# Optimization experiments

Hardware: AMD Instinct MI355X
Metric: run time of the kernel (lower is better)

Reference implementation:

```python
import jax, jax.numpy as jnp
import numpy as np

K = 4          # torus_dim (circles)
M = 6          # n_modes
GRID = 12      # grid_size for Laplacian eigenvalues
T = 2.0        # uniformity temperature
SPREAD_W = 1.0
B = 8192       # batch size


def _karmonic_weights():
    # lambda_n = 2 - 2 cos(2 pi n / N), n = 1..M; w = (lam - lam1)/(lam_max - lam1)
    n = np.arange(1, M + 1)
    lam = 2.0 - 2.0 * np.cos(2.0 * np.pi * n / GRID)
    w = (lam - lam[0]) / (lam.max() - lam[0])
    return jnp.asarray(w, dtype=jnp.float32)


def setup_inputs() -> dict:
    key = jax.random.key(0)
    k1, k2 = jax.random.split(key)
    angles = jax.random.normal(k1, (B, K), dtype=jnp.float32)
    fourier_embed = jax.random.normal(k2, (B, 2 * K * M), dtype=jnp.float32)
    return {"angles": angles, "fourier_embed": fourier_embed}


def reference(angles, fourier_embed):
    Bn = fourier_embed.shape[0]
    w = _karmonic_weights()
    # group by mode: (B, M, 2K)
    x = fourier_embed.reshape(Bn, M, 2 * K)
    eye = jnp.eye(Bn, dtype=bool)
    log_Bm1 = jnp.log(jnp.float32(Bn - 1))

    total_unif = jnp.float32(0.0)
    mode_unifs = []
    for n in range(M):  # fixed small structural loop over modes
        xn = x[:, n, :]                                   # (B, 2K)
        sq = jnp.sum(xn * xn, axis=1)                     # (B,)
        d2 = sq[:, None] + sq[None, :] - 2.0 * (xn @ xn.T)
        d2 = jnp.maximum(d2, 0.0)                         # cdist(...)**2, clamped >= 0
        neg = jnp.where(eye, -jnp.inf, -T * d2)           # exclude diagonal like masked_select
        unif_n = jnp.mean(jax.nn.logsumexp(neg, axis=1)) - log_Bm1
        mode_unifs.append(unif_n)
        total_unif = total_unif + w[n] * unif_n

    # circular decorrelation (spread) across circle pairs, vectorized over pairs
    mu = jnp.arctan2(jnp.mean(jnp.sin(angles), axis=0),
                     jnp.mean(jnp.cos(angles), axis=0))   # (K,) circular means
    s = jnp.sin(angles - mu[None, :])                     # (B, K)
    cov = (s.T @ s) / jnp.float32(Bn)                     # (K, K) = mean(s_i * s_j)
    var = jnp.diagonal(cov)                               # mean(s_i^2)
    den = jnp.sqrt(var[:, None] * var[None, :] + 1e-8)
    corr2 = (cov / den) ** 2
    iu = np.triu_indices(K, 1)                            # upper-triangle pairs i<j
    spread = jnp.mean(corr2[iu])

    total = total_unif + jnp.float32(SPREAD_W) * spread
    return total_unif, spread, total, jnp.stack(mode_unifs)
```

## Files before the change

### kernel.cpp

```cpp
#include <hip/hip_runtime.h>
#include <math.h>

constexpr int BN = 8192;
constexpr int MN = 6;

constexpr float TL    = 2.8853900817779268f;
constexpr float SCL_Z = 2.4022448795936154f;

typedef __bf16 bf16_t;
typedef bf16_t bf16x8 __attribute__((ext_vector_type(8)));
typedef float f32x4 __attribute__((ext_vector_type(4)));

union PK { bf16_t h[8]; uint4 u; };

__device__ __forceinline__ bf16x8 frag_of(uint4 u) {
    return __builtin_bit_cast(bf16x8, u);
}

__device__ __host__ __forceinline__ int midx(int a, int b) {
    return 8 * a - (a * (a - 1)) / 2 + (b - a);
}

__global__ __launch_bounds__(256) void prep_ang(const float* __restrict__ x,
                                                const float* __restrict__ ang,
                                                uint4* __restrict__ Ap,
                                                uint4* __restrict__ Bp,
                                                float* __restrict__ angp) {
    const int blk = blockIdx.x;
    const int tid = threadIdx.x;
    if (blk < 192) {
        int idx = blk * 256 + tid;
        int n = idx >> 13;
        int j = idx & (BN - 1);
        const float* p = x + (size_t)j * 48 + n * 8;

        PK zh, zl, a3, b3;
        float sq = 0.f;
#pragma unroll
        for (int k = 0; k < 8; ++k) {
            float v = p[k];
            sq = fmaf(v, v, sq);
            float z = SCL_Z * v;
            bf16_t h = (bf16_t)z;
            zh.h[k] = h;
            zl.h[k] = (bf16_t)(z - (float)h);
        }
        float s = -TL * sq;
        bf16_t sh = (bf16_t)s;
        bf16_t sl = (bf16_t)(s - (float)sh);
        bf16_t one = (bf16_t)1.0f, zero = (bf16_t)0.0f;
        a3.h[0] = one; a3.h[1] = one; a3.h[2] = sh;  a3.h[3] = sl;
        b3.h[0] = sh;  b3.h[1] = sl;  b3.h[2] = one; b3.h[3] = one;
#pragma unroll
        for (int k = 4; k < 8; ++k) { a3.h[k] = zero; b3.h[k] = zero; }

        size_t base = ((size_t)(n * 512 + (j >> 4))) * 64 + (j & 15);
        Ap[base +  0] = zh.u;
        Ap[base + 16] = zl.u;
        Ap[base + 32] = zh.u;
        Ap[base + 48] = a3.u;
        Bp[base +  0] = zh.u;
        Bp[base + 16] = zh.u;
        Bp[base + 32] = zl.u;
        Bp[base + 48] = b3.u;
    } else {
        const int i = (blk - 192) * 256 + tid;
        float v[8];
#pragma unroll
        for (int k = 0; k < 4; ++k) __sincosf(ang[i * 4 + k], &v[k], &v[4 + k]);
        float acc[44];
        int c = 0;
#pragma unroll
        for (int a = 0; a < 8; ++a)
#pragma unroll
            for (int bq = a; bq < 8; ++bq) acc[c++] = v[a] * v[bq];
#pragma unroll
        for (int a = 0; a < 8; ++a) acc[36 + a] = v[a];

#pragma unroll
        for (int q = 0; q < 44; ++q) {
            float s = acc[q];
            s += __shfl_xor(s, 1);  s += __shfl_xor(s, 2);
            s += __shfl_xor(s, 4);  s += __shfl_xor(s, 8);
            s += __shfl_xor(s, 16); s += __shfl_xor(s, 32);
            acc[q] = s;
        }
        __shared__ float sm[4][44];
        const int w = tid >> 6, lane = tid & 63;
        if (lane == 0)
#pragma unroll
            for (int q = 0; q < 44; ++q) sm[w][q] = acc[q];
        __syncthreads();
        if (tid < 44)
            angp[(blk - 192) * 44 + tid] =
                sm[0][tid] + sm[1][tid] + sm[2][tid] + sm[3][tid];
    }
}

__global__ __launch_bounds__(512, 6) void pair_mfma(const uint4* __restrict__ Ap,
                                                    const uint4* __restrict__ Bp,
                                                    float* __restrict__ lp) {
    const int tid  = threadIdx.x;
    const int lane = tid & 63;
    const int w    = __builtin_amdgcn_readfirstlane(tid >> 6);
    const int b    = blockIdx.x;
    const int n    = b >> 7;
    const int rb   = b & 127;
    const int rb4  = rb * 4;

    bf16x8 af[4];
#pragma unroll
    for (int t = 0; t < 4; ++t)
        af[t] = frag_of(Ap[((size_t)(n * 512 + rb4 + t)) * 64 + lane]);

    float racc[16];
#pragma unroll
    for (int q = 0; q < 16; ++q) racc[q] = 0.f;

    const uint4* bbase = Bp + ((size_t)n * 512) * 64 + lane;
    const f32x4 z4 = {0.f, 0.f, 0.f, 0.f};

    const int jt0 = w * 64, jt1 = jt0 + 64;
    uint4 b0 = bbase[(size_t)jt0 * 64];
    uint4 b1 = bbase[(size_t)(jt0 + 1) * 64];
    for (int jt = jt0; jt < jt1; jt += 2) {
        uint4 p0 = bbase[(size_t)(jt + 2) * 64];
        uint4 p1 = bbase[(size_t)(jt + 3) * 64];

        f32x4 d[4];
        bf16x8 bf = frag_of(b0);
#pragma unroll
        for (int t = 0; t < 4; ++t)
            d[t] = __builtin_amdgcn_mfma_f32_16x16x32_bf16(af[t], bf, z4, 0, 0, 0);
#pragma unroll
        for (int t = 0; t < 4; ++t)
#pragma unroll
            for (int r = 0; r < 4; ++r)
                racc[t * 4 + r] += __builtin_amdgcn_exp2f(d[t][r]);

        bf = frag_of(b1);
#pragma unroll
        for (int t = 0; t < 4; ++t)
            d[t] = __builtin_amdgcn_mfma_f32_16x16x32_bf16(af[t], bf, z4, 0, 0, 0);
#pragma unroll
        for (int t = 0; t < 4; ++t)
#pragma unroll
            for (int r = 0; r < 4; ++r)
                racc[t * 4 + r] += __builtin_amdgcn_exp2f(d[t][r]);

        b0 = p0; b1 = p1;
    }

    if ((rb4 >> 6) == w) {
        const int dd = (lane & 15) - 4 * (lane >> 4);
#pragma unroll
        for (int t = 0; t < 4; ++t) {
            bf16x8 bf = frag_of(bbase[(size_t)(rb4 + t) * 64]);
            f32x4 d = __builtin_amdgcn_mfma_f32_16x16x32_bf16(af[t], bf, z4, 0, 0, 0);
#pragma unroll
            for (int r = 0; r < 4; ++r)
                if (dd == r) racc[t * 4 + r] -= __builtin_amdgcn_exp2f(d[r]);
        }
    }

#pragma unroll
    for (int q = 0; q < 16; ++q) {
        float v = racc[q];
        v += __shfl_xor(v, 1);
        v += __shfl_xor(v, 2);
        v += __shfl_xor(v, 4);
        v += __shfl_xor(v, 8);
        racc[q] = v;
    }

    __shared__ float smem[8][64];
    if ((lane & 15) == 0) {
        int g = lane >> 4;
#pragma unroll
        for (int t = 0; t < 4; ++t)
#pragma unroll
            for (int r = 0; r < 4; ++r)
                smem[w][t * 16 + g * 4 + r] = racc[t * 4 + r];
    }
    __syncthreads();

    if (tid < 64) {
        float s = 0.f;
#pragma unroll
        for (int ww = 0; ww < 8; ++ww) s += smem[ww][tid];
        float lg = logf(s);
        lg += __shfl_xor(lg, 1);
        lg += __shfl_xor(lg, 2);
        lg += __shfl_xor(lg, 4);
        lg += __shfl_xor(lg, 8);
        lg += __shfl_xor(lg, 16);
        lg += __shfl_xor(lg, 32);
        if (tid == 0) lp[b] = lg;
    }
}

__global__ __launch_bounds__(1024) void final_asm(const float* __restrict__ angp,
                                                  const float* __restrict__ lp,
                                                  float* __restrict__ out) {
    const int tid = threadIdx.x;
    __shared__ float mom[44];
    __shared__ float lds[1024];
    __shared__ float spread_s;

    if (tid < 44) {
        float s = 0.f;
        for (int bk = 0; bk < 32; ++bk) s += angp[bk * 44 + tid];
        mom[tid] = s;
    }
    __syncthreads();

    if (tid == 0) {
        float sm[4], cm[4];
#pragma unroll
        for (int k = 0; k < 4; ++k) {
            float S = mom[36 + k], C = mom[40 + k];
            float hyp = sqrtf(S * S + C * C);
            sm[k] = S / hyp;
            cm[k] = C / hyp;
        }
        auto COV = [&](int k, int l) -> float {
            int ks = k < l ? k : l, kl = k < l ? l : k;
            float mss = mom[midx(ks, kl)];
            float msc_kl = mom[midx(k, l + 4)];
            float msc_lk = mom[midx(l, k + 4)];
            float mcc = mom[midx(ks + 4, kl + 4)];
            return (cm[k] * cm[l] * mss - cm[k] * sm[l] * msc_kl -
                    sm[k] * cm[l] * msc_lk + sm[k] * sm[l] * mcc) *
                   (1.0f / (float)BN);
        };
        float var[4] = {COV(0, 0), COV(1, 1), COV(2, 2), COV(3, 3)};
        float spread = 0.f;
        const int pk[6] = {0, 0, 0, 1, 1, 2};
        const int pl[6] = {1, 2, 3, 2, 3, 3};
#pragma unroll
        for (int p = 0; p < 6; ++p) {
            float cv = COV(pk[p], pl[p]);
            float den = sqrtf(var[pk[p]] * var[pl[p]] + 1e-8f);
            float cr = cv / den;
            spread += cr * cr;
        }
        spread_s = spread * (1.0f / 6.0f);
    }

    lds[tid] = (tid < 768) ? lp[tid] : 0.f;
    __syncthreads();
    for (int off = 64; off > 0; off >>= 1) {
        if ((tid & 127) < off && tid < 768) lds[tid] += lds[tid + off];
        __syncthreads();
    }

    if (tid == 0) {
        const float wgt[6] = {0.0f, 0.19615242270663188f, 0.4641016151377544f,
                              0.7320508075688773f, 0.9282032302755088f, 1.0f};
        const float logBm1 = logf((float)(BN - 1));
        float total_unif = 0.f, unif[6];
#pragma unroll
        for (int m = 0; m < 6; ++m) {
            unif[m] = lds[m * 128] * (1.0f / (float)BN) - logBm1;
            total_unif += wgt[m] * unif[m];
        }
        out[0] = total_unif;
        out[1] = spread_s;
        out[2] = total_unif + spread_s;
#pragma unroll
        for (int m = 0; m < 6; ++m) out[3 + m] = unif[m];
    }
}

extern "C" void kernel_launch(void* const* d_in, const int* in_sizes, int n_in,
                              void* d_out, int out_size, void* d_ws, size_t ws_size,
                              hipStream_t stream) {
    const float* angles  = (const float*)d_in[0];
    const float* fourier = (const float*)d_in[1];
    float* out = (float*)d_out;

    char* ws = (char*)d_ws;
    uint4* Bp   = (uint4*)(ws + 0);
    uint4* Ap   = (uint4*)(ws + 3145728);
    float* lp   = (float*)(ws + 6291456);
    float* angp = (float*)(ws + 6294528);

    prep_ang<<<dim3(224), dim3(256), 0, stream>>>(fourier, angles, Ap, Bp, angp);
    pair_mfma<<<dim3(MN * 128), dim3(512), 0, stream>>>(Ap, Bp, lp);
    final_asm<<<dim3(1), dim3(1024), 0, stream>>>(angp, lp, out);
}
```

Before: 60.37 us.

## Split pair kernel column range in half across two blocks, add log reduction kernel

Doubles the pair_mfma grid by giving each block half of the column tiles, interleaved with stride 16 across waves. Partial row sums go to a workspace, and a new log_red kernel adds the two halves, takes the log and reduces. The aim is better CU occupancy and load balance: 1536 blocks instead of 768, with launch bounds raised to 8 waves per SIMD. The cost is an extra kernel launch and a global round trip for the partial sums.

New measurement: 204.6 us. 3.39x slower.

```diff
diff --git a/kernel.cpp b/kernel.cpp
--- a/kernel.cpp
+++ b/kernel.cpp
@@ -97,16 +97,18 @@
     }
 }
 
-__global__ __launch_bounds__(512, 6) void pair_mfma(const uint4* __restrict__ Ap,
+__global__ __launch_bounds__(512, 8) void pair_mfma(const uint4* __restrict__ Ap,
                                                     const uint4* __restrict__ Bp,
-                                                    float* __restrict__ lp) {
+                                                    float* __restrict__ Sh) {
     const int tid  = threadIdx.x;
     const int lane = tid & 63;
     const int w    = __builtin_amdgcn_readfirstlane(tid >> 6);
     const int b    = blockIdx.x;
-    const int n    = b >> 7;
-    const int rb   = b & 127;
+    const int n    = b >> 8;
+    const int rb   = (b >> 1) & 127;
+    const int h    = b & 1;
     const int rb4  = rb * 4;
+    const int base = 2 * w + h;
 
     bf16x8 af[4];
 #pragma unroll
@@ -120,41 +122,41 @@
     const uint4* bbase = Bp + ((size_t)n * 512) * 64 + lane;
     const f32x4 z4 = {0.f, 0.f, 0.f, 0.f};
 
-    const int jt0 = w * 64, jt1 = jt0 + 64;
-    uint4 b0 = bbase[(size_t)jt0 * 64];
-    uint4 b1 = bbase[(size_t)(jt0 + 1) * 64];
-    for (int jt = jt0; jt < jt1; jt += 2) {
-        uint4 p0 = bbase[(size_t)(jt + 2) * 64];
-        uint4 p1 = bbase[(size_t)(jt + 3) * 64];
-
-        f32x4 d[4];
-        bf16x8 bf = frag_of(b0);
-#pragma unroll
-        for (int t = 0; t < 4; ++t)
-            d[t] = __builtin_amdgcn_mfma_f32_16x16x32_bf16(af[t], bf, z4, 0, 0, 0);
+    uint4 b0 = bbase[(size_t)base * 64];
+    uint4 b1 = bbase[(size_t)(base + 16) * 64];
+    for (int m = 0; m < 16; ++m) {
+        const int jtA = base + 32 * m;
+        uint4 p0 = bbase[(size_t)(jtA + 32) * 64];
+        uint4 p1 = bbase[(size_t)(jtA + 48) * 64];
+
+        bf16x8 bfA = frag_of(b0);
+        bf16x8 bfB = frag_of(b1);
+        f32x4 d0[4], d1[4];
+#pragma unroll
+        for (int t = 0; t < 4; ++t)
+            d0[t] = __builtin_amdgcn_mfma_f32_16x16x32_bf16(af[t], bfA, z4, 0, 0, 0);
+#pragma unroll
+        for (int t = 0; t < 4; ++t)
+            d1[t] = __builtin_amdgcn_mfma_f32_16x16x32_bf16(af[t], bfB, z4, 0, 0, 0);
 #pragma unroll
         for (int t = 0; t < 4; ++t)
 #pragma unroll
             for (int r = 0; r < 4; ++r)
-                racc[t * 4 + r] += __builtin_amdgcn_exp2f(d[t][r]);
-
-        bf = frag_of(b1);
-#pragma unroll
-        for (int t = 0; t < 4; ++t)
-            d[t] = __builtin_amdgcn_mfma_f32_16x16x32_bf16(af[t], bf, z4, 0, 0, 0);
+                racc[t * 4 + r] += __builtin_amdgcn_exp2f(d0[t][r]);
 #pragma unroll
         for (int t = 0; t < 4; ++t)
 #pragma unroll
             for (int r = 0; r < 4; ++r)
-                racc[t * 4 + r] += __builtin_amdgcn_exp2f(d[t][r]);
+                racc[t * 4 + r] += __builtin_amdgcn_exp2f(d1[t][r]);
 
         b0 = p0; b1 = p1;
     }
 
-    if ((rb4 >> 6) == w) {
-        const int dd = (lane & 15) - 4 * (lane >> 4);
-#pragma unroll
-        for (int t = 0; t < 4; ++t) {
+#pragma unroll
+    for (int t = 0; t < 4; ++t) {
+        const int rel = rb4 + t - base;
+        if (rel >= 0 && (rel & 15) == 0) {
+            const int dd = (lane & 15) - 4 * (lane >> 4);
             bf16x8 bf = frag_of(bbase[(size_t)(rb4 + t) * 64]);
             f32x4 d = __builtin_amdgcn_mfma_f32_16x16x32_bf16(af[t], bf, z4, 0, 0, 0);
 #pragma unroll
@@ -188,24 +190,38 @@
         float s = 0.f;
 #pragma unroll
         for (int ww = 0; ww < 8; ++ww) s += smem[ww][tid];
-        float lg = logf(s);
-        lg += __shfl_xor(lg, 1);
-        lg += __shfl_xor(lg, 2);
-        lg += __shfl_xor(lg, 4);
-        lg += __shfl_xor(lg, 8);
-        lg += __shfl_xor(lg, 16);
-        lg += __shfl_xor(lg, 32);
-        if (tid == 0) lp[b] = lg;
-    }
-}
-
-__global__ __launch_bounds__(1024) void final_asm(const float* __restrict__ angp,
-                                                  const float* __restrict__ lp,
-                                                  float* __restrict__ out) {
+        Sh[h * (MN * BN) + n * BN + rb * 64 + tid] = s;
+    }
+}
+
+__global__ __launch_bounds__(512) void log_red(const float* __restrict__ Sh,
+                                               float* __restrict__ lp) {
+    const int tid = threadIdx.x;
+    const int idx = blockIdx.x * 512 + tid;
+    float v = Sh[idx] + Sh[idx + MN * BN];
+    float lg = logf(v);
+    lg += __shfl_xor(lg, 1);
+    lg += __shfl_xor(lg, 2);
+    lg += __shfl_xor(lg, 4);
+    lg += __shfl_xor(lg, 8);
+    lg += __shfl_xor(lg, 16);
+    lg += __shfl_xor(lg, 32);
+    __shared__ float sm[8];
+    if ((tid & 63) == 0) sm[tid >> 6] = lg;
+    __syncthreads();
+    if (tid == 0) {
+        float s = 0.f;
+#pragma unroll
+        for (int i = 0; i < 8; ++i) s += sm[i];
+        lp[blockIdx.x] = s;
+    }
+}
+
+__global__ __launch_bounds__(64) void final_asm(const float* __restrict__ angp,
+                                                const float* __restrict__ lp,
+                                                float* __restrict__ out) {
     const int tid = threadIdx.x;
     __shared__ float mom[44];
-    __shared__ float lds[1024];
-    __shared__ float spread_s;
 
     if (tid < 44) {
         float s = 0.f;
@@ -244,29 +260,22 @@
             float cr = cv / den;
             spread += cr * cr;
         }
-        spread_s = spread * (1.0f / 6.0f);
-    }
-
-    lds[tid] = (tid < 768) ? lp[tid] : 0.f;
-    __syncthreads();
-    for (int off = 64; off > 0; off >>= 1) {
-        if ((tid & 127) < off && tid < 768) lds[tid] += lds[tid + off];
-        __syncthreads();
-    }
-
-    if (tid == 0) {
+        spread *= (1.0f / 6.0f);
+
         const float wgt[6] = {0.0f, 0.19615242270663188f, 0.4641016151377544f,
                               0.7320508075688773f, 0.9282032302755088f, 1.0f};
         const float logBm1 = logf((float)(BN - 1));
         float total_unif = 0.f, unif[6];
 #pragma unroll
         for (int m = 0; m < 6; ++m) {
-            unif[m] = lds[m * 128] * (1.0f / (float)BN) - logBm1;
+            float s = 0.f;
+            for (int i = 0; i < 16; ++i) s += lp[m * 16 + i];
+            unif[m] = s * (1.0f / (float)BN) - logBm1;
             total_unif += wgt[m] * unif[m];
         }
         out[0] = total_unif;
-        out[1] = spread_s;
-        out[2] = total_unif + spread_s;
+        out[1] = spread;
+        out[2] = total_unif + spread;
 #pragma unroll
         for (int m = 0; m < 6; ++m) out[3 + m] = unif[m];
     }
@@ -282,10 +291,12 @@
     char* ws = (char*)d_ws;
     uint4* Bp   = (uint4*)(ws + 0);
     uint4* Ap   = (uint4*)(ws + 3145728);
-    float* lp   = (float*)(ws + 6291456);
-    float* angp = (float*)(ws + 6294528);
+    float* Sh   = (float*)(ws + 6291456);
+    float* lp   = (float*)(ws + 6684672);
+    float* angp = (float*)(ws + 6685056);
 
     prep_ang<<<dim3(224), dim3(256), 0, stream>>>(fourier, angles, Ap, Bp, angp);
-    pair_mfma<<<dim3(MN * 128), dim3(512), 0, stream>>>(Ap, Bp, lp);
-    final_asm<<<dim3(1), dim3(1024), 0, stream>>>(angp, lp, out);
-}
+    pair_mfma<<<dim3(1536), dim3(512), 0, stream>>>(Ap, Bp, Sh);
+    log_red<<<dim3(96), dim3(512), 0, stream>>>(Sh, lp);
+    final_asm<<<dim3(1), dim3(64), 0, stream>>>(angp, lp, out);
+}
```
